# Kernel optimization log

Measured on AMD Instinct MI355X. Metric: run time of the kernel, lower is better.

Reference implementation:

```python
import jax, jax.numpy as jnp
import numpy as np

DIM = 1024
N_HEADS = 16
HEAD_DIM = DIM // N_HEADS


def setup_inputs() -> dict:
    key = jax.random.key(0)
    ks = jax.random.split(key, 5)
    s = 1.0 / np.sqrt(DIM)
    return {
        "x": jax.random.normal(ks[0], (2, 2048, DIM), dtype=jnp.float32),
        "w_qkv": jax.random.normal(ks[1], (DIM, 3 * DIM), dtype=jnp.float32) * s,
        "b_qkv": jnp.zeros((3 * DIM,), dtype=jnp.float32),
        "w_proj": jax.random.normal(ks[2], (DIM, DIM), dtype=jnp.float32) * s,
        "b_proj": jnp.zeros((DIM,), dtype=jnp.float32),
    }


def reference(x, w_qkv, b_qkv, w_proj, b_proj):
    B, T, C = x.shape
    qkv = x @ w_qkv + b_qkv                      # [B,T,3C]
    qkv = qkv.reshape(B, T, 3, N_HEADS, HEAD_DIM)
    q, k, v = qkv[:, :, 0], qkv[:, :, 1], qkv[:, :, 2]  # [B,T,H,D]
    scale = 1.0 / np.sqrt(HEAD_DIM)
    scores = jnp.einsum("bqhd,bkhd->bhqk", q, k) * scale  # [B,H,T,T]
    attn = jax.nn.softmax(scores, axis=-1)
    out = jnp.einsum("bhqk,bkhd->bqhd", attn, v)          # [B,T,H,D]
    out = out.reshape(B, T, C)
    return out @ w_proj + b_proj
```

## Files before the change

kernel.cpp:

```cpp
#include <hip/hip_runtime.h>

typedef unsigned short u16;
typedef unsigned int   u32;
typedef __bf16 bf16x8 __attribute__((ext_vector_type(8)));
typedef float  f32x4  __attribute__((ext_vector_type(4)));
typedef float  f32x16 __attribute__((ext_vector_type(16)));

#define TSEQ 2048
#define NHEAD 16
#define HDIM 64
#define CDIM 1024
#define N3   3072
#define MROWS 4096

__device__ __forceinline__ u16 f2bf(float f) {
    union { float f; u32 u; } v; v.f = f;
    u32 r = v.u + 0x7FFFu + ((v.u >> 16) & 1u);
    return (u16)(r >> 16);
}

__device__ __forceinline__ u32 pkbf(float a, float b) {
#if __has_builtin(__builtin_amdgcn_cvt_pk_bf16_f32)
    typedef __bf16 bf16x2 __attribute__((ext_vector_type(2)));
    bf16x2 t = __builtin_amdgcn_cvt_pk_bf16_f32(a, b);
    union { bf16x2 v; u32 u; } c; c.v = t; return c.u;
#else
    union { float f; u32 u; } ua, ub; ua.f = a; ub.f = b;
    u32 sel = 0x07060302, d;
    asm("v_perm_b32 %0, %1, %2, %3" : "=v"(d) : "v"(ub.u), "v"(ua.u), "v"(sel));
    return d;
#endif
}

__device__ __forceinline__ void gld16(const u16* g, u16* l) {
    __builtin_amdgcn_global_load_lds(
        (const __attribute__((address_space(1))) u32*)g,
        (__attribute__((address_space(3))) u32*)l, 16, 0, 0);
}

__global__ __launch_bounds__(256) void prep_kernel(const float* __restrict__ x,
                                                   const float* __restrict__ wqkv,
                                                   const float* __restrict__ wproj,
                                                   u16* __restrict__ Xb,
                                                   u16* __restrict__ oqkv, u16* __restrict__ oproj) {
    __shared__ float tile[32][33];
    const int bx = blockIdx.x;
    const int tid = threadIdx.x;
    if (bx < 4096) {
        int i = bx * 256 + tid;
        float4 v = reinterpret_cast<const float4*>(x)[i];
        ushort4 o;
        o.x = f2bf(v.x); o.y = f2bf(v.y); o.z = f2bf(v.z); o.w = f2bf(v.w);
        reinterpret_cast<ushort4*>(Xb)[i] = o;
        return;
    }
    int idx = bx - 4096;
    int bnx = idx & 127;
    int k0  = (idx >> 7) * 32;
    const float* in; u16* out; int N, n0;
    if (bnx < 96) { in = wqkv;  out = oqkv;  N = 3072; n0 = bnx * 32; }
    else          { in = wproj; out = oproj; N = 1024; n0 = (bnx - 96) * 32; }
    int tx = tid & 31, ty = tid >> 5;
#pragma unroll
    for (int i = 0; i < 4; i++)
        tile[ty + i * 8][tx] = in[(size_t)(k0 + ty + i * 8) * N + n0 + tx];
    __syncthreads();
#pragma unroll
    for (int i = 0; i < 4; i++)
        out[(size_t)(n0 + ty + i * 8) * 1024 + k0 + tx] = f2bf(tile[tx][ty + i * 8]);
}

#define QKV_STAGE(K0, AOFF, BOFF)                                                            \
    _Pragma("unroll") for (int s = 0; s < 2; s++) {                                          \
        int i = tid + s * 256;                                                               \
        int r = sr + s * 64;                                                                 \
        gld16(&A[(size_t)(row0 + r) * CDIM + (K0) + sc_], &smem[(AOFF) + i * 8]);            \
        gld16(&Bt[(size_t)(col0 + r) * CDIM + (K0) + sc_], &smem[(BOFF) + i * 8]);           \
    }

#define QKV_COMPUTE(AOFF, BOFF)                                                              \
    {                                                                                        \
        bf16x8 af[4], bfr[4];                                                                \
        _Pragma("unroll") for (int t = 0; t < 4; t++) {                                      \
            af[t]  = *reinterpret_cast<const bf16x8*>(&smem[(AOFF) + (wm + t * 16 + lr) * 32 + lq * 8]); \
            bfr[t] = *reinterpret_cast<const bf16x8*>(&smem[(BOFF) + (wn + t * 16 + lr) * 32 + lq * 8]); \
        }                                                                                    \
        _Pragma("unroll") for (int mt = 0; mt < 4; mt++)                                     \
            _Pragma("unroll") for (int nt = 0; nt < 4; nt++)                                 \
                acc[mt][nt] = __builtin_amdgcn_mfma_f32_16x16x32_bf16(af[mt], bfr[nt], acc[mt][nt], 0, 0, 0); \
    }

__global__ __launch_bounds__(256) void gemm_qkv(const u16* __restrict__ A, const u16* __restrict__ Bt,
                                                const float* __restrict__ bias, u16* __restrict__ Qf,
                                                u16* __restrict__ Kf, u16* __restrict__ Vf) {
    __shared__ __align__(16) u16 smem[16384];
    u16* Im = smem;
    const int tid  = threadIdx.x;
    const int lane = tid & 63;
    const int wave = tid >> 6;
    const int wm = (wave >> 1) * 64;
    const int wn = (wave & 1) * 64;
    const int row0 = blockIdx.x * 128;
    const int col0 = blockIdx.y * 128;
    const int lr = lane & 15;
    const int lq = lane >> 4;
    const float c2 = 0.125f * 1.44269504088896f;

    f32x4 acc[4][4];
#pragma unroll
    for (int i = 0; i < 4; i++)
#pragma unroll
        for (int j = 0; j < 4; j++) acc[i][j] = f32x4{0.f, 0.f, 0.f, 0.f};

    const int sr = tid >> 2, sc_ = (tid & 3) * 8;

    QKV_STAGE(0, 0, 4096);
    __syncthreads();
    for (int k0 = 0; k0 < CDIM - 64; k0 += 64) {
        QKV_STAGE(k0 + 32, 8192, 12288);
        QKV_COMPUTE(0, 4096);
        __syncthreads();
        QKV_STAGE(k0 + 64, 0, 4096);
        QKV_COMPUTE(8192, 12288);
        __syncthreads();
    }
    QKV_STAGE(992, 8192, 12288);
    QKV_COMPUTE(0, 4096);
    __syncthreads();
    QKV_COMPUTE(8192, 12288);
    __syncthreads();

    const int region = col0 >> 10;
    const int h_base = (col0 & 1023) >> 6;
#pragma unroll
    for (int mt = 0; mt < 4; mt++) {
#pragma unroll
        for (int nt = 0; nt < 4; nt++) {
            int n_local = wn + nt * 16 + lr;
            float bv = bias[col0 + n_local];
            int h_local = n_local >> 6;
            int d = n_local & 63;
#pragma unroll
            for (int r = 0; r < 4; r++) {
                int m_local = wm + mt * 16 + lq * 4 + r;
                float v = acc[mt][nt][r] + bv;
                if (region == 0) {
                    int qt_local = m_local >> 5, q31 = m_local & 31;
                    int kc = d >> 4, l5b = (d >> 3) & 1, j = d & 7;
                    int lc = (h_local * 4 + qt_local) * 4 + kc;
                    Im[lc * 512 + (l5b * 32 + q31) * 8 + j] = f2bf(v * c2);
                } else if (region == 1) {
                    int kb_local = m_local >> 6, tr = m_local & 63;
                    int kc = d >> 4, l5b = (d >> 3) & 1, j = d & 7;
                    int nt2 = tr >> 5, p31 = tr & 31;
                    int lc = (h_local * 2 + kb_local) * 8 + kc * 2 + nt2;
                    Im[lc * 512 + (l5b * 32 + p31) * 8 + j] = f2bf(v);
                } else {
                    int kb_local = m_local >> 6, tr = m_local & 63;
                    int cV = tr >> 4, dt2 = d >> 5, p31 = d & 31;
                    int l5b = (tr >> 2) & 1;
                    int j = ((tr >> 3) & 1) * 4 + (tr & 3);
                    int lc = (h_local * 2 + kb_local) * 8 + cV * 2 + dt2;
                    Im[lc * 512 + (l5b * 32 + p31) * 8 + j] = f2bf(v);
                }
            }
        }
    }
    __syncthreads();
    const int bq = row0 >> 11;
    const int qrow0 = row0 & 2047;
#pragma unroll
    for (int s = 0; s < 8; s++) {
        int slot = s * 256 + tid;
        int lc = slot >> 6, li = slot & 63;
        uint4 data = *reinterpret_cast<const uint4*>(&Im[slot * 8]);
        if (region == 0) {
            int h_local = lc >> 4, qt_local = (lc >> 2) & 3, kc = lc & 3;
            size_t off = ((size_t)((bq * 16 + h_base + h_local) * 64 + (qrow0 >> 5) + qt_local) * 4 + kc) * 512
                       + li * 8;
            *reinterpret_cast<uint4*>(Qf + off) = data;
        } else {
            int h_local = lc >> 4, kb_local = (lc >> 3) & 1, cit = lc & 7;
            size_t off = (size_t)((bq * 16 + h_base + h_local) * 32 + (qrow0 >> 6) + kb_local) * 4096
                       + cit * 512 + li * 8;
            *reinterpret_cast<uint4*>((region == 1 ? Kf : Vf) + off) = data;
        }
    }
}

#define PROJ_STAGE(K0, AOFF, BOFF)                                                           \
    _Pragma("unroll") for (int s = 0; s < 2; s++) {                                          \
        int i = tid + s * 256;                                                               \
        int kk = i >> 8, rr = (i >> 2) & 63, cc = i & 3;                                     \
        gld16(&A[(size_t)(row0 + rr) * CDIM + (K0) + kk * 32 + cc * 8], &smem[(AOFF) + i * 8]); \
    }                                                                                        \
    _Pragma("unroll") for (int s = 0; s < 4; s++) {                                          \
        int i = tid + s * 256;                                                               \
        int kk = i >> 9, rr = (i >> 2) & 127, cc = i & 3;                                    \
        gld16(&Bt[(size_t)(col0 + rr) * CDIM + (K0) + kk * 32 + cc * 8], &smem[(BOFF) + i * 8]); \
    }

#define PROJ_COMPUTE(AOFF, BOFF)                                                             \
    _Pragma("unroll") for (int kk = 0; kk < 2; kk++) {                                       \
        bf16x8 af[2], bfr[4];                                                                \
        _Pragma("unroll") for (int t = 0; t < 2; t++)                                        \
            af[t] = *reinterpret_cast<const bf16x8*>(&smem[(AOFF) + kk * 2048 + (wm + t * 16 + lr) * 32 + lq * 8]); \
        _Pragma("unroll") for (int t = 0; t < 4; t++)                                        \
            bfr[t] = *reinterpret_cast<const bf16x8*>(&smem[(BOFF) + kk * 4096 + (wn + t * 16 + lr) * 32 + lq * 8]); \
        _Pragma("unroll") for (int mt = 0; mt < 2; mt++)                                     \
            _Pragma("unroll") for (int nt = 0; nt < 4; nt++)                                 \
                acc[mt][nt] = __builtin_amdgcn_mfma_f32_16x16x32_bf16(af[mt], bfr[nt], acc[mt][nt], 0, 0, 0); \
    }

__global__ __launch_bounds__(256) void gemm_proj(const u16* __restrict__ A, const u16* __restrict__ Bt,
                                                 const float* __restrict__ bias, float* __restrict__ C) {
    __shared__ __align__(16) u16 smem[24576];
    const int tid  = threadIdx.x;
    const int lane = tid & 63;
    const int wave = tid >> 6;
    const int wm = (wave >> 1) * 32;
    const int wn = (wave & 1) * 64;
    const int row0 = blockIdx.x * 64;
    const int col0 = blockIdx.y * 128;
    const int lr = lane & 15;
    const int lq = lane >> 4;

    f32x4 acc[2][4];
#pragma unroll
    for (int i = 0; i < 2; i++)
#pragma unroll
        for (int j = 0; j < 4; j++) acc[i][j] = f32x4{0.f, 0.f, 0.f, 0.f};

    PROJ_STAGE(0, 0, 4096);
    __syncthreads();
    for (int k0 = 0; k0 < CDIM - 128; k0 += 128) {
        PROJ_STAGE(k0 + 64, 12288, 16384);
        PROJ_COMPUTE(0, 4096);
        __syncthreads();
        PROJ_STAGE(k0 + 128, 0, 4096);
        PROJ_COMPUTE(12288, 16384);
        __syncthreads();
    }
    PROJ_STAGE(960, 12288, 16384);
    PROJ_COMPUTE(0, 4096);
    __syncthreads();
    PROJ_COMPUTE(12288, 16384);

#pragma unroll
    for (int mt = 0; mt < 2; mt++) {
#pragma unroll
        for (int nt = 0; nt < 4; nt++) {
            int col = col0 + wn + nt * 16 + lr;
            float bv = bias[col];
#pragma unroll
            for (int r = 0; r < 4; r++) {
                int row = row0 + wm + mt * 16 + lq * 4 + r;
                C[(size_t)row * CDIM + col] = acc[mt][nt][r] + bv;
            }
        }
    }
}

__global__ __launch_bounds__(256, 1) void attn_kernel(const u16* __restrict__ Qf,
                                                      const u16* __restrict__ Kf,
                                                      const u16* __restrict__ Vf,
                                                      u16* __restrict__ AO) {
    const int id = blockIdx.x;
    const int bh = id & 31;
    const int qb = id >> 5;
    const int b = bh >> 4, h = bh & 15;
    const int tid = threadIdx.x, lane = tid & 63, wave = tid >> 6;
    const int l31 = lane & 31, l5 = lane >> 5;
    const int qt0 = qb * 8 + wave * 2;

    bf16x8 qa0[4], qa1[4];
    {
        const u16* qp = Qf + ((size_t)(bh * 64 + qt0) * 4) * 512 + lane * 8;
#pragma unroll
        for (int kc = 0; kc < 4; kc++) {
            qa0[kc] = *reinterpret_cast<const bf16x8*>(qp + kc * 512);
            qa1[kc] = *reinterpret_cast<const bf16x8*>(qp + 2048 + kc * 512);
        }
    }
    f32x16 o00, o01, o10, o11, zc;
#pragma unroll
    for (int i = 0; i < 16; i++) { o00[i] = 0.f; o01[i] = 0.f; o10[i] = 0.f; o11[i] = 0.f; zc[i] = 0.f; }
    float l0 = 0.f, l1 = 0.f;

    const u16* kcur = Kf + (size_t)bh * 32 * 4096 + lane * 8;
    const u16* vcur = Vf + (size_t)bh * 32 * 4096 + lane * 8;

    bf16x8 ka[8];
#pragma unroll
    for (int i = 0; i < 8; i++) ka[i] = *reinterpret_cast<const bf16x8*>(kcur + i * 512);

    for (int kb = 0; kb < 32; kb++) {
        f32x16 st00, st01, st10, st11;
        st00 = __builtin_amdgcn_mfma_f32_32x32x16_bf16(ka[0], qa0[0], zc, 0, 0, 0);
        st01 = __builtin_amdgcn_mfma_f32_32x32x16_bf16(ka[1], qa0[0], zc, 0, 0, 0);
        st10 = __builtin_amdgcn_mfma_f32_32x32x16_bf16(ka[0], qa1[0], zc, 0, 0, 0);
        st11 = __builtin_amdgcn_mfma_f32_32x32x16_bf16(ka[1], qa1[0], zc, 0, 0, 0);
#pragma unroll
        for (int kc = 1; kc < 4; kc++) {
            st00 = __builtin_amdgcn_mfma_f32_32x32x16_bf16(ka[kc * 2],     qa0[kc], st00, 0, 0, 0);
            st01 = __builtin_amdgcn_mfma_f32_32x32x16_bf16(ka[kc * 2 + 1], qa0[kc], st01, 0, 0, 0);
            st10 = __builtin_amdgcn_mfma_f32_32x32x16_bf16(ka[kc * 2],     qa1[kc], st10, 0, 0, 0);
            st11 = __builtin_amdgcn_mfma_f32_32x32x16_bf16(ka[kc * 2 + 1], qa1[kc], st11, 0, 0, 0);
        }
        bf16x8 vfr[8];
#pragma unroll
        for (int i = 0; i < 8; i++) vfr[i] = *reinterpret_cast<const bf16x8*>(vcur + i * 512);
        const u16* knext = kcur + (kb < 31 ? 4096 : 0);
#pragma unroll
        for (int i = 0; i < 8; i++) ka[i] = *reinterpret_cast<const bf16x8*>(knext + i * 512);
        kcur = knext;
        vcur += 4096;
        bf16x8 pa0[4], pa1[4];
        {
            float pe[16];
#pragma unroll
            for (int r = 0; r < 16; r++) { pe[r] = __builtin_amdgcn_exp2f(st00[r]); l0 += pe[r]; }
            union { bf16x8 v; u32 w[4]; } ua, ub;
#pragma unroll
            for (int j = 0; j < 4; j++) { ua.w[j] = pkbf(pe[2 * j], pe[2 * j + 1]); ub.w[j] = pkbf(pe[8 + 2 * j], pe[8 + 2 * j + 1]); }
            pa0[0] = ua.v; pa0[1] = ub.v;
#pragma unroll
            for (int r = 0; r < 16; r++) { pe[r] = __builtin_amdgcn_exp2f(st01[r]); l0 += pe[r]; }
#pragma unroll
            for (int j = 0; j < 4; j++) { ua.w[j] = pkbf(pe[2 * j], pe[2 * j + 1]); ub.w[j] = pkbf(pe[8 + 2 * j], pe[8 + 2 * j + 1]); }
            pa0[2] = ua.v; pa0[3] = ub.v;
#pragma unroll
            for (int r = 0; r < 16; r++) { pe[r] = __builtin_amdgcn_exp2f(st10[r]); l1 += pe[r]; }
#pragma unroll
            for (int j = 0; j < 4; j++) { ua.w[j] = pkbf(pe[2 * j], pe[2 * j + 1]); ub.w[j] = pkbf(pe[8 + 2 * j], pe[8 + 2 * j + 1]); }
            pa1[0] = ua.v; pa1[1] = ub.v;
#pragma unroll
            for (int r = 0; r < 16; r++) { pe[r] = __builtin_amdgcn_exp2f(st11[r]); l1 += pe[r]; }
#pragma unroll
            for (int j = 0; j < 4; j++) { ua.w[j] = pkbf(pe[2 * j], pe[2 * j + 1]); ub.w[j] = pkbf(pe[8 + 2 * j], pe[8 + 2 * j + 1]); }
            pa1[2] = ua.v; pa1[3] = ub.v;
        }
#pragma unroll
        for (int c = 0; c < 4; c++) {
            o00 = __builtin_amdgcn_mfma_f32_32x32x16_bf16(pa0[c], vfr[c * 2],     o00, 0, 0, 0);
            o01 = __builtin_amdgcn_mfma_f32_32x32x16_bf16(pa0[c], vfr[c * 2 + 1], o01, 0, 0, 0);
            o10 = __builtin_amdgcn_mfma_f32_32x32x16_bf16(pa1[c], vfr[c * 2],     o10, 0, 0, 0);
            o11 = __builtin_amdgcn_mfma_f32_32x32x16_bf16(pa1[c], vfr[c * 2 + 1], o11, 0, 0, 0);
        }
    }
    {
        float l = l0;
        l += __shfl_xor(l, 32);
        float linv = 1.0f / l;
        int q0 = qt0 * 32;
#pragma unroll
        for (int reg = 0; reg < 16; reg++) {
            int qrow = (reg & 3) + 8 * (reg >> 2) + 4 * l5;
            float li = __shfl(linv, qrow);
            AO[(size_t)(b * TSEQ + q0 + qrow) * CDIM + h * 64 + l31]      = f2bf(o00[reg] * li);
            AO[(size_t)(b * TSEQ + q0 + qrow) * CDIM + h * 64 + 32 + l31] = f2bf(o01[reg] * li);
        }
    }
    {
        float l = l1;
        l += __shfl_xor(l, 32);
        float linv = 1.0f / l;
        int q0 = (qt0 + 1) * 32;
#pragma unroll
        for (int reg = 0; reg < 16; reg++) {
            int qrow = (reg & 3) + 8 * (reg >> 2) + 4 * l5;
            float li = __shfl(linv, qrow);
            AO[(size_t)(b * TSEQ + q0 + qrow) * CDIM + h * 64 + l31]      = f2bf(o10[reg] * li);
            AO[(size_t)(b * TSEQ + q0 + qrow) * CDIM + h * 64 + 32 + l31] = f2bf(o11[reg] * li);
        }
    }
}

extern "C" void kernel_launch(void* const* d_in, const int* in_sizes, int n_in,
                              void* d_out, int out_size, void* d_ws, size_t ws_size,
                              hipStream_t stream) {
    const float* x      = (const float*)d_in[0];
    const float* w_qkv  = (const float*)d_in[1];
    const float* b_qkv  = (const float*)d_in[2];
    const float* w_proj = (const float*)d_in[3];
    const float* b_proj = (const float*)d_in[4];
    float* out = (float*)d_out;

    u16* ws     = (u16*)d_ws;
    u16* Xb     = ws;
    u16* Wqkvt  = Xb + 4194304;
    u16* Wprojt = Wqkvt + 3145728;
    u16* Qf     = Wprojt + 1048576;
    u16* Kf     = Qf + 4194304;
    u16* Vf     = Kf + 4194304;
    u16* AO     = Vf + 4194304;

    prep_kernel<<<8192, 256, 0, stream>>>(x, w_qkv, w_proj, Xb, Wqkvt, Wprojt);
    gemm_qkv<<<dim3(32, 24), 256, 0, stream>>>(Xb, Wqkvt, b_qkv, Qf, Kf, Vf);
    attn_kernel<<<256, 256, 0, stream>>>(Qf, Kf, Vf, AO);
    gemm_proj<<<dim3(64, 8), 256, 0, stream>>>(AO, Wprojt, b_proj, out);
}
```

Before: 170.6 us.

## Split attention key range across two wave groups and merge partials in LDS

The attention block grows to 512 threads. Each of the two wave groups handles half of the key blocks for the same query tiles, and the partial O accumulators and row sums are combined through shared memory before the normalised output is written. This doubles the waves per CU, which is meant to hide latency in the attention kernel, which was previously limited to 256 launched blocks with 4 waves each. The change also adds s_setprio around the MFMA sections, loads V at the top of the loop, and splits the row-sum accumulation across four partial sums. The cost is an LDS reduction, a block-wide barrier and higher register pressure under the 512-thread launch bound.

After: 184.8 us. 1.08x slower.

```diff
diff --git a/kernel.cpp b/kernel.cpp
--- a/kernel.cpp
+++ b/kernel.cpp
@@ -261,17 +261,21 @@
     }
 }
 
-__global__ __launch_bounds__(256, 1) void attn_kernel(const u16* __restrict__ Qf,
+__global__ __launch_bounds__(512, 1) void attn_kernel(const u16* __restrict__ Qf,
                                                       const u16* __restrict__ Kf,
                                                       const u16* __restrict__ Vf,
                                                       u16* __restrict__ AO) {
+    __shared__ __align__(16) float Ol[4][16][64][4];
+    __shared__ float Ll[4][64][2];
     const int id = blockIdx.x;
     const int bh = id & 31;
-    const int qb = id >> 5;
+    const int qc = id >> 5;
     const int b = bh >> 4, h = bh & 15;
     const int tid = threadIdx.x, lane = tid & 63, wave = tid >> 6;
+    const int wp   = wave & 3;
+    const int half = wave >> 2;
     const int l31 = lane & 31, l5 = lane >> 5;
-    const int qt0 = qb * 8 + wave * 2;
+    const int qt0 = qc * 8 + wp * 2;
 
     bf16x8 qa0[4], qa1[4];
     {
@@ -285,17 +289,23 @@
     f32x16 o00, o01, o10, o11, zc;
 #pragma unroll
     for (int i = 0; i < 16; i++) { o00[i] = 0.f; o01[i] = 0.f; o10[i] = 0.f; o11[i] = 0.f; zc[i] = 0.f; }
-    float l0 = 0.f, l1 = 0.f;
-
-    const u16* kcur = Kf + (size_t)bh * 32 * 4096 + lane * 8;
-    const u16* vcur = Vf + (size_t)bh * 32 * 4096 + lane * 8;
+    float la0[4], la1[4];
+#pragma unroll
+    for (int i = 0; i < 4; i++) { la0[i] = 0.f; la1[i] = 0.f; }
+
+    const u16* kcur = Kf + ((size_t)bh * 32 + half * 16) * 4096 + lane * 8;
+    const u16* vcur = Vf + ((size_t)bh * 32 + half * 16) * 4096 + lane * 8;
 
     bf16x8 ka[8];
 #pragma unroll
     for (int i = 0; i < 8; i++) ka[i] = *reinterpret_cast<const bf16x8*>(kcur + i * 512);
 
-    for (int kb = 0; kb < 32; kb++) {
+    for (int kb = 0; kb < 16; kb++) {
+        bf16x8 vfr[8];
+#pragma unroll
+        for (int i = 0; i < 8; i++) vfr[i] = *reinterpret_cast<const bf16x8*>(vcur + i * 512);
         f32x16 st00, st01, st10, st11;
+        __builtin_amdgcn_s_setprio(1);
         st00 = __builtin_amdgcn_mfma_f32_32x32x16_bf16(ka[0], qa0[0], zc, 0, 0, 0);
         st01 = __builtin_amdgcn_mfma_f32_32x32x16_bf16(ka[1], qa0[0], zc, 0, 0, 0);
         st10 = __builtin_amdgcn_mfma_f32_32x32x16_bf16(ka[0], qa1[0], zc, 0, 0, 0);
@@ -307,10 +317,8 @@
             st10 = __builtin_amdgcn_mfma_f32_32x32x16_bf16(ka[kc * 2],     qa1[kc], st10, 0, 0, 0);
             st11 = __builtin_amdgcn_mfma_f32_32x32x16_bf16(ka[kc * 2 + 1], qa1[kc], st11, 0, 0, 0);
         }
-        bf16x8 vfr[8];
-#pragma unroll
-        for (int i = 0; i < 8; i++) vfr[i] = *reinterpret_cast<const bf16x8*>(vcur + i * 512);
-        const u16* knext = kcur + (kb < 31 ? 4096 : 0);
+        __builtin_amdgcn_s_setprio(0);
+        const u16* knext = kcur + (kb < 15 ? 4096 : 0);
 #pragma unroll
         for (int i = 0; i < 8; i++) ka[i] = *reinterpret_cast<const bf16x8*>(knext + i * 512);
         kcur = knext;
@@ -318,28 +326,29 @@
         bf16x8 pa0[4], pa1[4];
         {
             float pe[16];
-#pragma unroll
-            for (int r = 0; r < 16; r++) { pe[r] = __builtin_amdgcn_exp2f(st00[r]); l0 += pe[r]; }
             union { bf16x8 v; u32 w[4]; } ua, ub;
+#pragma unroll
+            for (int r = 0; r < 16; r++) { pe[r] = __builtin_amdgcn_exp2f(st00[r]); la0[r & 3] += pe[r]; }
 #pragma unroll
             for (int j = 0; j < 4; j++) { ua.w[j] = pkbf(pe[2 * j], pe[2 * j + 1]); ub.w[j] = pkbf(pe[8 + 2 * j], pe[8 + 2 * j + 1]); }
             pa0[0] = ua.v; pa0[1] = ub.v;
 #pragma unroll
-            for (int r = 0; r < 16; r++) { pe[r] = __builtin_amdgcn_exp2f(st01[r]); l0 += pe[r]; }
+            for (int r = 0; r < 16; r++) { pe[r] = __builtin_amdgcn_exp2f(st01[r]); la0[r & 3] += pe[r]; }
 #pragma unroll
             for (int j = 0; j < 4; j++) { ua.w[j] = pkbf(pe[2 * j], pe[2 * j + 1]); ub.w[j] = pkbf(pe[8 + 2 * j], pe[8 + 2 * j + 1]); }
             pa0[2] = ua.v; pa0[3] = ub.v;
 #pragma unroll
-            for (int r = 0; r < 16; r++) { pe[r] = __builtin_amdgcn_exp2f(st10[r]); l1 += pe[r]; }
+            for (int r = 0; r < 16; r++) { pe[r] = __builtin_amdgcn_exp2f(st10[r]); la1[r & 3] += pe[r]; }
 #pragma unroll
             for (int j = 0; j < 4; j++) { ua.w[j] = pkbf(pe[2 * j], pe[2 * j + 1]); ub.w[j] = pkbf(pe[8 + 2 * j], pe[8 + 2 * j + 1]); }
             pa1[0] = ua.v; pa1[1] = ub.v;
 #pragma unroll
-            for (int r = 0; r < 16; r++) { pe[r] = __builtin_amdgcn_exp2f(st11[r]); l1 += pe[r]; }
+            for (int r = 0; r < 16; r++) { pe[r] = __builtin_amdgcn_exp2f(st11[r]); la1[r & 3] += pe[r]; }
 #pragma unroll
             for (int j = 0; j < 4; j++) { ua.w[j] = pkbf(pe[2 * j], pe[2 * j + 1]); ub.w[j] = pkbf(pe[8 + 2 * j], pe[8 + 2 * j + 1]); }
             pa1[2] = ua.v; pa1[3] = ub.v;
         }
+        __builtin_amdgcn_s_setprio(1);
 #pragma unroll
         for (int c = 0; c < 4; c++) {
             o00 = __builtin_amdgcn_mfma_f32_32x32x16_bf16(pa0[c], vfr[c * 2],     o00, 0, 0, 0);
@@ -347,7 +356,41 @@
             o10 = __builtin_amdgcn_mfma_f32_32x32x16_bf16(pa1[c], vfr[c * 2],     o10, 0, 0, 0);
             o11 = __builtin_amdgcn_mfma_f32_32x32x16_bf16(pa1[c], vfr[c * 2 + 1], o11, 0, 0, 0);
         }
-    }
+        __builtin_amdgcn_s_setprio(0);
+    }
+
+    float l0 = (la0[0] + la0[1]) + (la0[2] + la0[3]);
+    float l1 = (la1[0] + la1[1]) + (la1[2] + la1[3]);
+    if (half == 1) {
+#pragma unroll
+        for (int g = 0; g < 4; g++) {
+            *reinterpret_cast<f32x4*>(&Ol[wp][g][lane][0])      = f32x4{o00[4*g], o00[4*g+1], o00[4*g+2], o00[4*g+3]};
+            *reinterpret_cast<f32x4*>(&Ol[wp][g + 4][lane][0])  = f32x4{o01[4*g], o01[4*g+1], o01[4*g+2], o01[4*g+3]};
+            *reinterpret_cast<f32x4*>(&Ol[wp][g + 8][lane][0])  = f32x4{o10[4*g], o10[4*g+1], o10[4*g+2], o10[4*g+3]};
+            *reinterpret_cast<f32x4*>(&Ol[wp][g + 12][lane][0]) = f32x4{o11[4*g], o11[4*g+1], o11[4*g+2], o11[4*g+3]};
+        }
+        Ll[wp][lane][0] = l0;
+        Ll[wp][lane][1] = l1;
+    }
+    __syncthreads();
+    if (half == 1) return;
+    l0 += Ll[wp][lane][0];
+    l1 += Ll[wp][lane][1];
+#pragma unroll
+    for (int g = 0; g < 4; g++) {
+        f32x4 a0 = *reinterpret_cast<const f32x4*>(&Ol[wp][g][lane][0]);
+        f32x4 a1 = *reinterpret_cast<const f32x4*>(&Ol[wp][g + 4][lane][0]);
+        f32x4 a2 = *reinterpret_cast<const f32x4*>(&Ol[wp][g + 8][lane][0]);
+        f32x4 a3 = *reinterpret_cast<const f32x4*>(&Ol[wp][g + 12][lane][0]);
+#pragma unroll
+        for (int j = 0; j < 4; j++) {
+            o00[4*g + j] += a0[j];
+            o01[4*g + j] += a1[j];
+            o10[4*g + j] += a2[j];
+            o11[4*g + j] += a3[j];
+        }
+    }
+
     {
         float l = l0;
         l += __shfl_xor(l, 32);
@@ -397,6 +440,6 @@
 
     prep_kernel<<<8192, 256, 0, stream>>>(x, w_qkv, w_proj, Xb, Wqkvt, Wprojt);
     gemm_qkv<<<dim3(32, 24), 256, 0, stream>>>(Xb, Wqkvt, b_qkv, Qf, Kf, Vf);
-    attn_kernel<<<256, 256, 0, stream>>>(Qf, Kf, Vf, AO);
+    attn_kernel<<<256, 512, 0, stream>>>(Qf, Kf, Vf, AO);
     gemm_proj<<<dim3(64, 8), 256, 0, stream>>>(AO, Wprojt, b_proj, out);
 }
```

## Deepen GEMM load pipeline with partial vmcnt waits and raw barriers

Applied to the files above, without the earlier changes.

Restructures the QKV and projection GEMM main loops so two LDS stages are in flight at once. Each compute step waits only for the older stage using partial s_waitcnt vmcnt counts and a bare s_barrier, instead of a full __syncthreads. The aim is to keep async global-to-LDS loads overlapping MFMA compute rather than draining all memory traffic at every barrier. The hand-set vmcnt values must match the exact number of loads each stage issues, or the kernel races.

Result: no change. 171.3 us (+0.4%).

```diff
diff --git a/kernel.cpp b/kernel.cpp
--- a/kernel.cpp
+++ b/kernel.cpp
@@ -37,6 +37,12 @@
         (const __attribute__((address_space(1))) u32*)g,
         (__attribute__((address_space(3))) u32*)l, 16, 0, 0);
 }
+
+#define VMW4()  asm volatile("s_waitcnt vmcnt(4)" ::: "memory")
+#define VMW6()  asm volatile("s_waitcnt vmcnt(6)" ::: "memory")
+#define VMW0()  asm volatile("s_waitcnt vmcnt(0)" ::: "memory")
+#define LGKM0() asm volatile("s_waitcnt lgkmcnt(0)" ::: "memory")
+#define FBAR()  asm volatile("s_barrier" ::: "memory")
 
 __global__ __launch_bounds__(256) void prep_kernel(const float* __restrict__ x,
                                                    const float* __restrict__ wqkv,
@@ -115,18 +121,21 @@
     const int sr = tid >> 2, sc_ = (tid & 3) * 8;
 
     QKV_STAGE(0, 0, 4096);
-    __syncthreads();
-    for (int k0 = 0; k0 < CDIM - 64; k0 += 64) {
-        QKV_STAGE(k0 + 32, 8192, 12288);
+    QKV_STAGE(32, 8192, 12288);
+    for (int it = 0; it < 15; it++) {
+        int k0 = it * 64;
+        VMW4(); FBAR();
         QKV_COMPUTE(0, 4096);
-        __syncthreads();
+        LGKM0(); FBAR();
         QKV_STAGE(k0 + 64, 0, 4096);
+        VMW4(); FBAR();
         QKV_COMPUTE(8192, 12288);
-        __syncthreads();
-    }
-    QKV_STAGE(992, 8192, 12288);
+        LGKM0(); FBAR();
+        QKV_STAGE(k0 + 96, 8192, 12288);
+    }
+    VMW4(); FBAR();
     QKV_COMPUTE(0, 4096);
-    __syncthreads();
+    VMW0(); FBAR();
     QKV_COMPUTE(8192, 12288);
     __syncthreads();
 
@@ -232,18 +241,21 @@
         for (int j = 0; j < 4; j++) acc[i][j] = f32x4{0.f, 0.f, 0.f, 0.f};
 
     PROJ_STAGE(0, 0, 4096);
-    __syncthreads();
-    for (int k0 = 0; k0 < CDIM - 128; k0 += 128) {
-        PROJ_STAGE(k0 + 64, 12288, 16384);
+    PROJ_STAGE(64, 12288, 16384);
+    for (int it = 0; it < 7; it++) {
+        int k0 = it * 128;
+        VMW6(); FBAR();
         PROJ_COMPUTE(0, 4096);
-        __syncthreads();
+        LGKM0(); FBAR();
         PROJ_STAGE(k0 + 128, 0, 4096);
+        VMW6(); FBAR();
         PROJ_COMPUTE(12288, 16384);
-        __syncthreads();
-    }
-    PROJ_STAGE(960, 12288, 16384);
+        LGKM0(); FBAR();
+        PROJ_STAGE(k0 + 192, 12288, 16384);
+    }
+    VMW6(); FBAR();
     PROJ_COMPUTE(0, 4096);
-    __syncthreads();
+    VMW0(); FBAR();
     PROJ_COMPUTE(12288, 16384);
 
 #pragma unroll
```
